# Performance work log

Measured on AMD Instinct MI355X. Metric: run time of the kernel, lower is better.

Reference implementation:

```python
import jax, jax.numpy as jnp
import numpy as np

INPUT_DIM = 128
HIDDEN_DIM = 128
WINDOW_SIZE = 256
BLOCK_SIZE = 256
BATCH = 8
SEQ = 8192


def setup_inputs() -> dict:
    key = jax.random.key(0)
    ks = jax.random.split(key, 7)
    s = 1.0 / np.sqrt(INPUT_DIM)
    return {
        "x": jax.random.normal(ks[0], (BATCH, SEQ, INPUT_DIM), dtype=jnp.float32),
        "Wq": jax.random.normal(ks[1], (HIDDEN_DIM, INPUT_DIM), dtype=jnp.float32) * s,
        "bq": jax.random.normal(ks[2], (HIDDEN_DIM,), dtype=jnp.float32) * s,
        "Wk": jax.random.normal(ks[3], (HIDDEN_DIM, INPUT_DIM), dtype=jnp.float32) * s,
        "bk": jax.random.normal(ks[4], (HIDDEN_DIM,), dtype=jnp.float32) * s,
        "Wv": jax.random.normal(ks[5], (HIDDEN_DIM, INPUT_DIM), dtype=jnp.float32) * s,
        "bv": jax.random.normal(ks[6], (HIDDEN_DIM,), dtype=jnp.float32) * s,
    }


def reference(x, Wq, bq, Wk, bk, Wv, bv):
    B, S, D = x.shape
    bs, w = BLOCK_SIZE, WINDOW_SIZE
    nb = S // bs
    halo = w - 1
    W = bs + 2 * halo  # per-block K/V window width

    q = x @ Wq.T + bq  # [B,S,H]
    k = x @ Wk.T + bk
    v = x @ Wv.T + bv

    # Zero-pad K/V by halo on both sides. Since there is NO softmax, padded
    # zero keys give zero scores and padded zero values contribute zero —
    # this exactly reproduces the torch code's clamped window slicing.
    k_pad = jnp.pad(k, ((0, 0), (halo, halo), (0, 0)))
    v_pad = jnp.pad(v, ((0, 0), (halo, halo), (0, 0)))

    # Gather overlapping windows: [B, nb, W, H]
    starts = jnp.arange(nb) * bs  # window start in padded coords
    idx = starts[:, None] + jnp.arange(W)[None, :]  # [nb, W]
    k_win = k_pad[:, idx, :]
    v_win = v_pad[:, idx, :]

    q_blk = q.reshape(B, nb, bs, -1)  # [B, nb, bs, H]

    scale = 1.0 / jnp.sqrt(jnp.float32(D))
    attn = jnp.einsum('bnqh,bnkh->bnqk', q_blk, k_win) * scale  # no softmax
    out = jnp.einsum('bnqk,bnkh->bnqh', attn, v_win)
    return out.reshape(B, S, -1)
```

## Files before the change

kernel.cpp:

```cpp
#include <hip/hip_runtime.h>
#include <stdint.h>


#define B_ 8
#define S_ 8192

using bf16x8 = __attribute__((ext_vector_type(8))) short;
using s16x4  = __attribute__((ext_vector_type(4))) short;
using f32x16 = __attribute__((ext_vector_type(16))) float;

__device__ __forceinline__ short f2bf(float f) {
  union { float f; uint32_t u; } v; v.f = f;
  uint32_t r = v.u + 0x7fffu + ((v.u >> 16) & 1u);
  return (short)(r >> 16);
}
__device__ __forceinline__ float bf2f(short s) {
  union { uint32_t u; float f; } v; v.u = ((uint32_t)(uint16_t)s) << 16;
  return v.f;
}

#define LDW 136

__global__ __launch_bounds__(256) void proj_kernel(
    const float* __restrict__ x,
    const float* __restrict__ Wq, const float* __restrict__ bq,
    const float* __restrict__ Wk, const float* __restrict__ bk,
    const float* __restrict__ Wv, const float* __restrict__ bv,
    short* __restrict__ qb, short* __restrict__ ktb, short* __restrict__ vtb,
    short* __restrict__ kedge, short* __restrict__ vedge)
{
  __shared__ short wl[128 * LDW];

  const int tid  = threadIdx.x;
  const int lane = tid & 63;
  const int wv   = tid >> 6;
  const int c    = lane & 31;
  const int hl   = lane >> 5;
  const int r0   = blockIdx.x * 128;
  const int b    = r0 >> 13;
  const int s0   = r0 & (S_ - 1);

  bf16x8 afrag[8];
  {
    const float* xrow = x + (size_t)(r0 + wv * 32 + c) * 128 + hl * 8;
    #pragma unroll
    for (int kst = 0; kst < 8; ++kst) {
      const float4* p = (const float4*)(xrow + kst * 16);
      float4 f0 = p[0], f1 = p[1];
      bf16x8 a;
      a[0] = f2bf(f0.x); a[1] = f2bf(f0.y); a[2] = f2bf(f0.z); a[3] = f2bf(f0.w);
      a[4] = f2bf(f1.x); a[5] = f2bf(f1.y); a[6] = f2bf(f1.z); a[7] = f2bf(f1.w);
      afrag[kst] = a;
    }
  }

  auto stageW = [&](const float* W) {
    #pragma unroll
    for (int it = 0; it < 16; ++it) {
      int l  = it * 256 + tid;
      int n  = l >> 5;
      int k4 = (l & 31) << 2;
      const float4 f = *(const float4*)(W + n * 128 + k4);
      s16x4 o;
      o[0] = f2bf(f.x); o[1] = f2bf(f.y); o[2] = f2bf(f.z); o[3] = f2bf(f.w);
      *(s16x4*)(wl + n * LDW + k4) = o;
    }
  };

  auto gemm = [&](const float* bias, f32x16* acc) {
    #pragma unroll
    for (int nt = 0; nt < 4; ++nt) {
      float bvv = bias[nt * 32 + c];
      #pragma unroll
      for (int i = 0; i < 16; ++i) acc[nt][i] = bvv;
    }
    #pragma unroll
    for (int kst = 0; kst < 8; ++kst) {
      #pragma unroll
      for (int nt = 0; nt < 4; ++nt) {
        bf16x8 bb = *(const bf16x8*)(wl + (nt * 32 + c) * LDW + kst * 16 + hl * 8);
        acc[nt] = __builtin_amdgcn_mfma_f32_32x32x16_bf16(afrag[kst], bb, acc[nt], 0, 0, 0);
      }
    }
  };

  auto writeTransposedLDS = [&](f32x16* acc) {
    #pragma unroll
    for (int nt = 0; nt < 4; ++nt) {
      int d = nt * 32 + c;
      #pragma unroll
      for (int g = 0; g < 4; ++g) {
        #pragma unroll
        for (int p = 0; p < 2; ++p) {
          int reg = g * 4 + p * 2;
          int sl  = wv * 32 + g * 8 + hl * 4 + p * 2;
          uint32_t pk = (uint32_t)(uint16_t)f2bf(acc[nt][reg]) |
                        ((uint32_t)(uint16_t)f2bf(acc[nt][reg + 1]) << 16);
          *(uint32_t*)(wl + d * LDW + sl) = pk;
        }
      }
    }
  };

  auto storeTransposed = [&](short* dst) {
    #pragma unroll
    for (int it = 0; it < 8; ++it) {
      int l  = it * 256 + tid;
      int d  = l >> 4;
      int s8 = (l & 15) << 3;
      bf16x8 vv = *(const bf16x8*)(wl + d * LDW + s8);
      *(bf16x8*)(dst + ((size_t)b * 128 + d) * S_ + s0 + s8) = vv;
    }
  };

  auto storeEdge = [&](short* edst) {
    if (tid < 128) {
      size_t eo = ((size_t)b * 32 + (s0 >> 8)) * 256;
      if ((s0 & 255) == 0) edst[eo + tid]       = wl[tid * LDW + 0];
      else                 edst[eo + 128 + tid] = wl[tid * LDW + 127];
    }
  };

  stageW(Wq);
  __syncthreads();
  {
    f32x16 acc[4];
    gemm(bq, acc);
    __syncthreads();
    #pragma unroll
    for (int nt = 0; nt < 4; ++nt) {
      #pragma unroll
      for (int reg = 0; reg < 16; ++reg) {
        int row = (reg & 3) + 8 * (reg >> 2) + 4 * hl;
        wl[(wv * 32 + row) * LDW + nt * 32 + c] = f2bf(acc[nt][reg]);
      }
    }
    __syncthreads();
    #pragma unroll
    for (int it = 0; it < 8; ++it) {
      int l  = it * 256 + tid;
      int s  = l >> 4;
      int d8 = (l & 15) << 3;
      bf16x8 vv = *(const bf16x8*)(wl + s * LDW + d8);
      *(bf16x8*)(qb + (size_t)(r0 + s) * 128 + d8) = vv;
    }
  }
  __syncthreads();

  stageW(Wk);
  __syncthreads();
  {
    f32x16 acc[4];
    gemm(bk, acc);
    __syncthreads();
    writeTransposedLDS(acc);
    __syncthreads();
    storeTransposed(ktb);
    storeEdge(kedge);
  }
  __syncthreads();

  stageW(Wv);
  __syncthreads();
  {
    f32x16 acc[4];
    gemm(bv, acc);
    __syncthreads();
    writeTransposedLDS(acc);
    __syncthreads();
    storeTransposed(vtb);
    storeEdge(vedge);
  }
}

__global__ __launch_bounds__(512) void chunkc_kernel(
    const short* __restrict__ ktb, const short* __restrict__ vtb,
    float* __restrict__ Cb)
{
  const int tid  = threadIdx.x;
  const int lane = tid & 63;
  const int wv   = tid >> 6;
  const int c    = lane & 31;
  const int hl   = lane >> 5;
  const int b    = blockIdx.x >> 5;
  const int n    = blockIdx.x & 31;
  const int s0   = n * 256;

  const short* ap = vtb + ((size_t)b * 128 + (wv >> 1) * 32 + c) * S_ + s0 + hl * 8;
  const short* bp = ktb + ((size_t)b * 128 + (wv & 1) * 64 + c) * S_ + s0 + hl * 8;

  f32x16 acc[2];
  #pragma unroll
  for (int t = 0; t < 2; ++t)
    #pragma unroll
    for (int i = 0; i < 16; ++i) acc[t][i] = 0.f;

  #pragma unroll
  for (int kst = 0; kst < 16; ++kst) {
    bf16x8 a  = *(const bf16x8*)(ap + kst * 16);
    bf16x8 b0 = *(const bf16x8*)(bp + kst * 16);
    bf16x8 b1 = *(const bf16x8*)(bp + (size_t)32 * S_ + kst * 16);
    acc[0] = __builtin_amdgcn_mfma_f32_32x32x16_bf16(a, b0, acc[0], 0, 0, 0);
    acc[1] = __builtin_amdgcn_mfma_f32_32x32x16_bf16(a, b1, acc[1], 0, 0, 0);
  }

  float* Cp = Cb + ((size_t)(b * 32 + n)) * 16384;
  #pragma unroll
  for (int t = 0; t < 2; ++t) {
    #pragma unroll
    for (int reg = 0; reg < 16; ++reg) {
      int row = (reg & 3) + 8 * (reg >> 2) + 4 * hl;
      Cp[((wv >> 1) * 32 + row) * 128 + (wv & 1) * 64 + t * 32 + c] = acc[t][reg];
    }
  }
}

#define LDM 136

__global__ __launch_bounds__(512) void attn_kernel(
    const short* __restrict__ qb, const float* __restrict__ Cb,
    const short* __restrict__ kedge, const short* __restrict__ vedge,
    float* __restrict__ out)
{
  __shared__ __align__(16) short m_l[128 * LDM];
  __shared__ __align__(16) float opat[8 * 32 * 36];

  const int tid  = threadIdx.x;
  const int lane = tid & 63;
  const int wv   = tid >> 6;
  const int c    = lane & 31;
  const int hl   = lane >> 5;
  const int b    = blockIdx.x >> 5;
  const int n    = blockIdx.x & 31;

  const int h  = tid >> 2;
  const int dq = (tid & 3) << 5;

  float m[32];
  #pragma unroll
  for (int i = 0; i < 32; ++i) m[i] = 0.f;

  const float* Cbase = Cb + (size_t)b * 32 * 16384;
  #pragma unroll
  for (int dn = -1; dn <= 1; ++dn) {
    int nn = n + dn;
    if (nn < 0 || nn > 31) continue;
    const float* Cp = Cbase + (size_t)nn * 16384 + h * 128 + dq;
    #pragma unroll
    for (int i4 = 0; i4 < 8; ++i4) {
      float4 f = *(const float4*)(Cp + i4 * 4);
      m[i4 * 4 + 0] += f.x; m[i4 * 4 + 1] += f.y;
      m[i4 * 4 + 2] += f.z; m[i4 * 4 + 3] += f.w;
    }
  }
  if (n > 0) {
    const short* ke = kedge + ((size_t)(b * 32 + n - 1)) * 256;
    const short* ve = vedge + ((size_t)(b * 32 + n - 1)) * 256;
    float vs = bf2f(ve[h]);
    #pragma unroll
    for (int i8 = 0; i8 < 4; ++i8) {
      bf16x8 kr = *(const bf16x8*)(ke + dq + i8 * 8);
      #pragma unroll
      for (int j = 0; j < 8; ++j) m[i8 * 8 + j] -= vs * bf2f(kr[j]);
    }
  }
  if (n < 31) {
    const short* ke = kedge + ((size_t)(b * 32 + n + 1)) * 256 + 128;
    const short* ve = vedge + ((size_t)(b * 32 + n + 1)) * 256 + 128;
    float vs = bf2f(ve[h]);
    #pragma unroll
    for (int i8 = 0; i8 < 4; ++i8) {
      bf16x8 kr = *(const bf16x8*)(ke + dq + i8 * 8);
      #pragma unroll
      for (int j = 0; j < 8; ++j) m[i8 * 8 + j] -= vs * bf2f(kr[j]);
    }
  }
  const float scale = 0.08838834764831845f;
  #pragma unroll
  for (int i = 0; i < 16; ++i) {
    uint32_t pk = (uint32_t)(uint16_t)f2bf(m[2 * i] * scale) |
                  ((uint32_t)(uint16_t)f2bf(m[2 * i + 1] * scale) << 16);
    *(uint32_t*)(m_l + h * LDM + dq + 2 * i) = pk;
  }

  bf16x8 qf[8];
  {
    const short* q0p = qb + ((size_t)b * S_ + n * 256 + wv * 32 + c) * 128 + hl * 8;
    #pragma unroll
    for (int kst = 0; kst < 8; ++kst) qf[kst] = *(const bf16x8*)(q0p + kst * 16);
  }
  __syncthreads();

  f32x16 oacc[4];
  #pragma unroll
  for (int nt = 0; nt < 4; ++nt)
    #pragma unroll
    for (int i = 0; i < 16; ++i) oacc[nt][i] = 0.f;

  #pragma unroll
  for (int kst = 0; kst < 8; ++kst) {
    #pragma unroll
    for (int nt = 0; nt < 4; ++nt) {
      bf16x8 bb = *(const bf16x8*)(m_l + (nt * 32 + c) * LDM + kst * 16 + hl * 8);
      oacc[nt] = __builtin_amdgcn_mfma_f32_32x32x16_bf16(qf[kst], bb, oacc[nt], 0, 0, 0);
    }
  }

  float* patch = opat + wv * (32 * 36);
  float* outb  = out + ((size_t)b * S_ + n * 256 + wv * 32) * 128;
  #pragma unroll
  for (int nt = 0; nt < 4; ++nt) {
    #pragma unroll
    for (int reg = 0; reg < 16; ++reg) {
      int row = (reg & 3) + 8 * (reg >> 2) + 4 * hl;
      patch[row * 36 + c] = oacc[nt][reg];
    }
    #pragma unroll
    for (int p = 0; p < 4; ++p) {
      int row = p * 8 + (lane >> 3);
      float4 vv = *(const float4*)(patch + row * 36 + (lane & 7) * 4);
      *(float4*)(outb + (size_t)row * 128 + nt * 32 + (lane & 7) * 4) = vv;
    }
  }
}

extern "C" void kernel_launch(void* const* d_in, const int* in_sizes, int n_in,
                              void* d_out, int out_size, void* d_ws, size_t ws_size,
                              hipStream_t stream) {
  const float* x  = (const float*)d_in[0];
  const float* Wq = (const float*)d_in[1];
  const float* bq = (const float*)d_in[2];
  const float* Wk = (const float*)d_in[3];
  const float* bk = (const float*)d_in[4];
  const float* Wv = (const float*)d_in[5];
  const float* bv = (const float*)d_in[6];
  float* out = (float*)d_out;

  const size_t elems = (size_t)B_ * S_ * 128;
  short* qb    = (short*)d_ws;
  short* ktb   = qb + elems;
  short* vtb   = ktb + elems;
  float* Cb    = (float*)(vtb + elems);
  short* kedge = (short*)(Cb + (size_t)8 * 32 * 16384);
  short* vedge = kedge + (size_t)8 * 32 * 256;

  proj_kernel<<<512, 256, 0, stream>>>(x, Wq, bq, Wk, bk, Wv, bv,
                                       qb, ktb, vtb, kedge, vedge);
  chunkc_kernel<<<256, 512, 0, stream>>>(ktb, vtb, Cb);
  attn_kernel<<<256, 512, 0, stream>>>(qb, Cb, kedge, vedge, out);
}
```

Measured before the change: 135.6 us.

## Fuse chunk V^T K product into projection kernel and drop separate chunk kernel

The separate kernel that reread K^T and V^T from global memory to form per-256-row chunk V^T·K matrices is removed. The projection kernel now keeps the K and V tiles in two LDS buffers and computes a per-128-row partial V^T·K product with MFMA, writing twice as many fp32 partials. The attention kernel sums six half-chunk partials instead of three full ones, using coalesced float4 reads, and the edge-correction loop is remapped to match. This saves a kernel launch and a global reread of K/V, at the cost of more LDS in the projection kernel and more partial-matrix traffic.

```diff
diff --git a/kernel.cpp b/kernel.cpp
--- a/kernel.cpp
+++ b/kernel.cpp
@@ -27,9 +27,11 @@
     const float* __restrict__ Wk, const float* __restrict__ bk,
     const float* __restrict__ Wv, const float* __restrict__ bv,
     short* __restrict__ qb, short* __restrict__ ktb, short* __restrict__ vtb,
-    short* __restrict__ kedge, short* __restrict__ vedge)
+    short* __restrict__ kedge, short* __restrict__ vedge,
+    float* __restrict__ Cpart)
 {
-  __shared__ short wl[128 * LDW];
+  __shared__ short wlA[128 * LDW];
+  __shared__ short wlB[128 * LDW];
 
   const int tid  = threadIdx.x;
   const int lane = tid & 63;
@@ -54,7 +56,7 @@
     }
   }
 
-  auto stageW = [&](const float* W) {
+  auto stageW = [&](const float* W, short* wl) {
     #pragma unroll
     for (int it = 0; it < 16; ++it) {
       int l  = it * 256 + tid;
@@ -67,7 +69,7 @@
     }
   };
 
-  auto gemm = [&](const float* bias, f32x16* acc) {
+  auto gemm = [&](const float* bias, f32x16* acc, const short* wl) {
     #pragma unroll
     for (int nt = 0; nt < 4; ++nt) {
       float bvv = bias[nt * 32 + c];
@@ -84,7 +86,7 @@
     }
   };
 
-  auto writeTransposedLDS = [&](f32x16* acc) {
+  auto writeTransposedLDS = [&](f32x16* acc, short* wl) {
     #pragma unroll
     for (int nt = 0; nt < 4; ++nt) {
       int d = nt * 32 + c;
@@ -102,7 +104,7 @@
     }
   };
 
-  auto storeTransposed = [&](short* dst) {
+  auto storeTransposed = [&](short* dst, const short* wl) {
     #pragma unroll
     for (int it = 0; it < 8; ++it) {
       int l  = it * 256 + tid;
@@ -113,7 +115,7 @@
     }
   };
 
-  auto storeEdge = [&](short* edst) {
+  auto storeEdge = [&](short* edst, const short* wl) {
     if (tid < 128) {
       size_t eo = ((size_t)b * 32 + (s0 >> 8)) * 256;
       if ((s0 & 255) == 0) edst[eo + tid]       = wl[tid * LDW + 0];
@@ -121,18 +123,71 @@
     }
   };
 
-  stageW(Wq);
+  stageW(Wk, wlA);
   __syncthreads();
   {
     f32x16 acc[4];
-    gemm(bq, acc);
-    __syncthreads();
+    gemm(bk, acc, wlA);
+    __syncthreads();
+    writeTransposedLDS(acc, wlA);
+    __syncthreads();
+    storeTransposed(ktb, wlA);
+    storeEdge(kedge, wlA);
+  }
+
+  stageW(Wv, wlB);
+  __syncthreads();
+  {
+    f32x16 acc[4];
+    gemm(bv, acc, wlB);
+    __syncthreads();
+    writeTransposedLDS(acc, wlB);
+    __syncthreads();
+    storeTransposed(vtb, wlB);
+    storeEdge(vedge, wlB);
+  }
+
+  {
+    f32x16 cacc[4];
+    #pragma unroll
+    for (int nt = 0; nt < 4; ++nt)
+      #pragma unroll
+      for (int i = 0; i < 16; ++i) cacc[nt][i] = 0.f;
+
+    #pragma unroll
+    for (int kst = 0; kst < 8; ++kst) {
+      bf16x8 a = *(const bf16x8*)(wlB + (wv * 32 + c) * LDW + kst * 16 + hl * 8);
+      #pragma unroll
+      for (int nt = 0; nt < 4; ++nt) {
+        bf16x8 bb = *(const bf16x8*)(wlA + (nt * 32 + c) * LDW + kst * 16 + hl * 8);
+        cacc[nt] = __builtin_amdgcn_mfma_f32_32x32x16_bf16(a, bb, cacc[nt], 0, 0, 0);
+      }
+    }
+
+    float* Cp = Cpart + ((size_t)b * 64 + (s0 >> 7)) * 16384;
     #pragma unroll
     for (int nt = 0; nt < 4; ++nt) {
       #pragma unroll
       for (int reg = 0; reg < 16; ++reg) {
         int row = (reg & 3) + 8 * (reg >> 2) + 4 * hl;
-        wl[(wv * 32 + row) * LDW + nt * 32 + c] = f2bf(acc[nt][reg]);
+        Cp[(wv * 32 + row) * 128 + nt * 32 + c] = cacc[nt][reg];
+      }
+    }
+  }
+  __syncthreads();
+
+  stageW(Wq, wlA);
+  __syncthreads();
+  {
+    f32x16 acc[4];
+    gemm(bq, acc, wlA);
+    __syncthreads();
+    #pragma unroll
+    for (int nt = 0; nt < 4; ++nt) {
+      #pragma unroll
+      for (int reg = 0; reg < 16; ++reg) {
+        int row = (reg & 3) + 8 * (reg >> 2) + 4 * hl;
+        wlA[(wv * 32 + row) * LDW + nt * 32 + c] = f2bf(acc[nt][reg]);
       }
     }
     __syncthreads();
@@ -141,42 +196,22 @@
       int l  = it * 256 + tid;
       int s  = l >> 4;
       int d8 = (l & 15) << 3;
-      bf16x8 vv = *(const bf16x8*)(wl + s * LDW + d8);
+      bf16x8 vv = *(const bf16x8*)(wlA + s * LDW + d8);
       *(bf16x8*)(qb + (size_t)(r0 + s) * 128 + d8) = vv;
     }
   }
-  __syncthreads();
-
-  stageW(Wk);
-  __syncthreads();
-  {
-    f32x16 acc[4];
-    gemm(bk, acc);
-    __syncthreads();
-    writeTransposedLDS(acc);
-    __syncthreads();
-    storeTransposed(ktb);
-    storeEdge(kedge);
-  }
-  __syncthreads();
-
-  stageW(Wv);
-  __syncthreads();
-  {
-    f32x16 acc[4];
-    gemm(bv, acc);
-    __syncthreads();
-    writeTransposedLDS(acc);
-    __syncthreads();
-    storeTransposed(vtb);
-    storeEdge(vedge);
-  }
-}
-
-__global__ __launch_bounds__(512) void chunkc_kernel(
-    const short* __restrict__ ktb, const short* __restrict__ vtb,
-    float* __restrict__ Cb)
+}
+
+#define LDM 136
+
+__global__ __launch_bounds__(512) void attn_kernel(
+    const short* __restrict__ qb, const float* __restrict__ Cpart,
+    const short* __restrict__ kedge, const short* __restrict__ vedge,
+    float* __restrict__ out)
 {
+  __shared__ __align__(16) short m_l[128 * LDM];
+  __shared__ __align__(16) float opat[8 * 32 * 36];
+
   const int tid  = threadIdx.x;
   const int lane = tid & 63;
   const int wv   = tid >> 6;
@@ -184,103 +219,59 @@
   const int hl   = lane >> 5;
   const int b    = blockIdx.x >> 5;
   const int n    = blockIdx.x & 31;
-  const int s0   = n * 256;
-
-  const short* ap = vtb + ((size_t)b * 128 + (wv >> 1) * 32 + c) * S_ + s0 + hl * 8;
-  const short* bp = ktb + ((size_t)b * 128 + (wv & 1) * 64 + c) * S_ + s0 + hl * 8;
-
-  f32x16 acc[2];
-  #pragma unroll
-  for (int t = 0; t < 2; ++t)
-    #pragma unroll
-    for (int i = 0; i < 16; ++i) acc[t][i] = 0.f;
-
-  #pragma unroll
-  for (int kst = 0; kst < 16; ++kst) {
-    bf16x8 a  = *(const bf16x8*)(ap + kst * 16);
-    bf16x8 b0 = *(const bf16x8*)(bp + kst * 16);
-    bf16x8 b1 = *(const bf16x8*)(bp + (size_t)32 * S_ + kst * 16);
-    acc[0] = __builtin_amdgcn_mfma_f32_32x32x16_bf16(a, b0, acc[0], 0, 0, 0);
-    acc[1] = __builtin_amdgcn_mfma_f32_32x32x16_bf16(a, b1, acc[1], 0, 0, 0);
-  }
-
-  float* Cp = Cb + ((size_t)(b * 32 + n)) * 16384;
-  #pragma unroll
-  for (int t = 0; t < 2; ++t) {
-    #pragma unroll
-    for (int reg = 0; reg < 16; ++reg) {
-      int row = (reg & 3) + 8 * (reg >> 2) + 4 * hl;
-      Cp[((wv >> 1) * 32 + row) * 128 + (wv & 1) * 64 + t * 32 + c] = acc[t][reg];
-    }
-  }
-}
-
-#define LDM 136
-
-__global__ __launch_bounds__(512) void attn_kernel(
-    const short* __restrict__ qb, const float* __restrict__ Cb,
-    const short* __restrict__ kedge, const short* __restrict__ vedge,
-    float* __restrict__ out)
-{
-  __shared__ __align__(16) short m_l[128 * LDM];
-  __shared__ __align__(16) float opat[8 * 32 * 36];
-
-  const int tid  = threadIdx.x;
-  const int lane = tid & 63;
-  const int wv   = tid >> 6;
-  const int c    = lane & 31;
-  const int hl   = lane >> 5;
-  const int b    = blockIdx.x >> 5;
-  const int n    = blockIdx.x & 31;
-
-  const int h  = tid >> 2;
-  const int dq = (tid & 3) << 5;
 
   float m[32];
   #pragma unroll
   for (int i = 0; i < 32; ++i) m[i] = 0.f;
 
-  const float* Cbase = Cb + (size_t)b * 32 * 16384;
-  #pragma unroll
-  for (int dn = -1; dn <= 1; ++dn) {
-    int nn = n + dn;
-    if (nn < 0 || nn > 31) continue;
-    const float* Cp = Cbase + (size_t)nn * 16384 + h * 128 + dq;
+  const float* Cb0 = Cpart + (size_t)b * 64 * 16384;
+  #pragma unroll
+  for (int e = 0; e < 6; ++e) {
+    int hj = 2 * n - 2 + e;
+    if (hj < 0 || hj >= 64) continue;
+    const float4* Cp = (const float4*)(Cb0 + (size_t)hj * 16384);
     #pragma unroll
     for (int i4 = 0; i4 < 8; ++i4) {
-      float4 f = *(const float4*)(Cp + i4 * 4);
+      float4 f = Cp[i4 * 512 + tid];
       m[i4 * 4 + 0] += f.x; m[i4 * 4 + 1] += f.y;
       m[i4 * 4 + 2] += f.z; m[i4 * 4 + 3] += f.w;
     }
   }
+
+  const int d0 = (tid & 31) << 2;
   if (n > 0) {
     const short* ke = kedge + ((size_t)(b * 32 + n - 1)) * 256;
     const short* ve = vedge + ((size_t)(b * 32 + n - 1)) * 256;
-    float vs = bf2f(ve[h]);
-    #pragma unroll
-    for (int i8 = 0; i8 < 4; ++i8) {
-      bf16x8 kr = *(const bf16x8*)(ke + dq + i8 * 8);
-      #pragma unroll
-      for (int j = 0; j < 8; ++j) m[i8 * 8 + j] -= vs * bf2f(kr[j]);
+    float k0 = bf2f(ke[d0]),     k1 = bf2f(ke[d0 + 1]);
+    float k2 = bf2f(ke[d0 + 2]), k3 = bf2f(ke[d0 + 3]);
+    #pragma unroll
+    for (int i4 = 0; i4 < 8; ++i4) {
+      float vs = bf2f(ve[i4 * 16 + (tid >> 5)]);
+      m[i4 * 4 + 0] -= vs * k0; m[i4 * 4 + 1] -= vs * k1;
+      m[i4 * 4 + 2] -= vs * k2; m[i4 * 4 + 3] -= vs * k3;
     }
   }
   if (n < 31) {
     const short* ke = kedge + ((size_t)(b * 32 + n + 1)) * 256 + 128;
     const short* ve = vedge + ((size_t)(b * 32 + n + 1)) * 256 + 128;
-    float vs = bf2f(ve[h]);
-    #pragma unroll
-    for (int i8 = 0; i8 < 4; ++i8) {
-      bf16x8 kr = *(const bf16x8*)(ke + dq + i8 * 8);
-      #pragma unroll
-      for (int j = 0; j < 8; ++j) m[i8 * 8 + j] -= vs * bf2f(kr[j]);
-    }
-  }
+    float k0 = bf2f(ke[d0]),     k1 = bf2f(ke[d0 + 1]);
+    float k2 = bf2f(ke[d0 + 2]), k3 = bf2f(ke[d0 + 3]);
+    #pragma unroll
+    for (int i4 = 0; i4 < 8; ++i4) {
+      float vs = bf2f(ve[i4 * 16 + (tid >> 5)]);
+      m[i4 * 4 + 0] -= vs * k0; m[i4 * 4 + 1] -= vs * k1;
+      m[i4 * 4 + 2] -= vs * k2; m[i4 * 4 + 3] -= vs * k3;
+    }
+  }
+
   const float scale = 0.08838834764831845f;
   #pragma unroll
-  for (int i = 0; i < 16; ++i) {
-    uint32_t pk = (uint32_t)(uint16_t)f2bf(m[2 * i] * scale) |
-                  ((uint32_t)(uint16_t)f2bf(m[2 * i + 1] * scale) << 16);
-    *(uint32_t*)(m_l + h * LDM + dq + 2 * i) = pk;
+  for (int i4 = 0; i4 < 8; ++i4) {
+    int h = i4 * 16 + (tid >> 5);
+    s16x4 o;
+    o[0] = f2bf(m[i4 * 4 + 0] * scale); o[1] = f2bf(m[i4 * 4 + 1] * scale);
+    o[2] = f2bf(m[i4 * 4 + 2] * scale); o[3] = f2bf(m[i4 * 4 + 3] * scale);
+    *(s16x4*)(m_l + h * LDM + d0) = o;
   }
 
   bf16x8 qf[8];
@@ -340,12 +331,11 @@
   short* qb    = (short*)d_ws;
   short* ktb   = qb + elems;
   short* vtb   = ktb + elems;
-  float* Cb    = (float*)(vtb + elems);
-  short* kedge = (short*)(Cb + (size_t)8 * 32 * 16384);
+  float* Cpart = (float*)(vtb + elems);
+  short* kedge = (short*)(Cpart + (size_t)8 * 64 * 16384);
   short* vedge = kedge + (size_t)8 * 32 * 256;
 
   proj_kernel<<<512, 256, 0, stream>>>(x, Wq, bq, Wk, bk, Wv, bv,
-                                       qb, ktb, vtb, kedge, vedge);
-  chunkc_kernel<<<256, 512, 0, stream>>>(ktb, vtb, Cb);
-  attn_kernel<<<256, 512, 0, stream>>>(qb, Cb, kedge, vedge, out);
-}
+                                       qb, ktb, vtb, kedge, vedge, Cpart);
+  attn_kernel<<<256, 512, 0, stream>>>(qb, Cpart, kedge, vedge, out);
+}
```

Measured after the change: 129.4 us. 1.05x faster.
